# Optimization experiments

Hardware: AMD Instinct MI355X
Metric: run time of the kernel (lower is better)

## Reference

```python
import jax, jax.numpy as jnp
import numpy as np

S, V, H = 32, 16, 8            # hidden_scalars, hidden_vectors, num_heads
N, E = 10000, 100000           # nodes, edges
NRB, RH = 16, 64               # radial basis, radial MLP hidden
TH = S + 3 * V                 # packed irreps width (80)
WNUM = S * S + V * S + S * V + 2 * V * V  # TP weight_numel = 2560


def setup_inputs() -> dict:
    key = jax.random.key(0)
    ks = jax.random.split(key, 16)
    inp = {}
    inp["node_features"] = jax.random.normal(ks[0], (N, TH), jnp.float32)
    inp["edge_index"] = jax.random.randint(ks[1], (2, E), 0, N)
    inp["edge_sh"] = jax.random.normal(ks[2], (E, 4), jnp.float32)
    inp["edge_radial"] = jax.random.uniform(ks[3], (E, NRB), dtype=jnp.float32)
    inp["edge_envelope"] = jax.random.uniform(ks[4], (E,), dtype=jnp.float32)
    # radial MLP
    inp["W1"] = jax.random.normal(ks[5], (NRB, RH), jnp.float32) / np.sqrt(NRB)
    inp["b1"] = jnp.zeros((RH,), jnp.float32)
    inp["W2"] = jax.random.normal(ks[6], (RH, WNUM), jnp.float32) / np.sqrt(RH)
    inp["b2"] = jnp.zeros((WNUM,), jnp.float32)
    # attention query/key nets (scalar channels only)
    inp["Wq"] = jax.random.normal(ks[7], (S, H), jnp.float32) / np.sqrt(S)
    inp["bq"] = jnp.zeros((H,), jnp.float32)
    inp["Wk"] = jax.random.normal(ks[8], (S, H), jnp.float32) / np.sqrt(S)
    inp["bk"] = jnp.zeros((H,), jnp.float32)
    # equivariant linears (per-irrep channel mixing, e3nn style, no bias)
    inp["Wout_s"] = jax.random.normal(ks[9], (S, S), jnp.float32)
    inp["Wout_v"] = jax.random.normal(ks[10], (V, V), jnp.float32)
    inp["Wg_s"] = jax.random.normal(ks[11], (S, S + V), jnp.float32)
    inp["Wg_v"] = jax.random.normal(ks[12], (V, V), jnp.float32)
    # equivariant batch norm params
    inp["bn_ws"] = jnp.ones((S,), jnp.float32)
    inp["bn_bs"] = jnp.zeros((S,), jnp.float32)
    inp["bn_wv"] = jnp.ones((V,), jnp.float32)
    return inp


def _forward(node_features, edge_sh, edge_radial, edge_envelope,
             W1, b1, W2, b2, Wq, bq, Wk, bk,
             Wout_s, Wout_v, Wg_s, Wg_v, bn_ws, bn_bs, bn_wv, src, dst):
    # --- per-edge TP weights from radial MLP -> (E, WNUM), the big tensor ---
    tp_w = jax.nn.silu(edge_radial @ W1 + b1) @ W2 + b2
    offs = np.cumsum([0, S * S, V * S, S * V, V * V, V * V])
    WA = tp_w[:, offs[0]:offs[1]].reshape(-1, S, S)  # 0e x 0e -> 0e
    WB = tp_w[:, offs[1]:offs[2]].reshape(-1, V, S)  # 1o x 1o -> 0e
    WC = tp_w[:, offs[2]:offs[3]].reshape(-1, S, V)  # 0e x 1o -> 1o
    WD = tp_w[:, offs[3]:offs[4]].reshape(-1, V, V)  # 1o x 0e -> 1o
    WE = tp_w[:, offs[4]:offs[5]].reshape(-1, V, V)  # 1o x 1o -> 1o (cross)

    # --- gather source features, split irreps ---
    s_src = node_features[src, :S]                       # (E, S)
    v_src = node_features[src, S:].reshape(-1, V, 3)     # (E, V, 3)
    y0 = edge_sh[:, 0:1]                                 # (E, 1) l=0
    y1 = edge_sh[:, 1:4]                                 # (E, 3) l=1

    a0 = 1.0 / np.sqrt(S + V)       # path normalization, 0e output
    a1 = 1.0 / np.sqrt(S + 2 * V)   # path normalization, 1o output

    dot = (v_src * y1[:, None, :]).sum(-1) / np.sqrt(3.0)          # (E, V)
    msg_s = a0 * (jnp.einsum('es,esk->ek', s_src * y0, WA)
                  + jnp.einsum('ev,evk->ek', dot, WB))             # (E, S)
    crs = jnp.cross(v_src, y1[:, None, :]) / np.sqrt(2.0)          # (E, V, 3)
    msg_v = a1 * (jnp.einsum('es,ec,esk->ekc', s_src, y1, WC)
                  + jnp.einsum('evc,evk->ekc', v_src * y0[:, :, None], WD)
                  + jnp.einsum('evc,evk->ekc', crs, WE))           # (E, V, 3)
    messages = jnp.concatenate([msg_s, msg_v.reshape(-1, 3 * V)], axis=-1)

    # --- scatter-softmax attention over incoming edges per destination ---
    q = node_features[dst, :S] @ Wq + bq                 # (E, H)
    k = msg_s @ Wk + bk                                  # (E, H)
    logits = (q * k).sum(-1) / np.sqrt(H) + jnp.log(edge_envelope + 1e-8)
    mx = jax.ops.segment_max(logits, dst, num_segments=N)
    ex = jnp.exp(logits - mx[dst])
    den = jax.ops.segment_sum(ex, dst, num_segments=N)
    attn = ex / (den[dst] + 1e-8)                        # (E,)

    agg = jax.ops.segment_sum(attn[:, None] * messages, dst, num_segments=N)

    # --- equivariant output linear ---
    agg_s = agg[:, :S] @ Wout_s / np.sqrt(S)
    agg_v = jnp.einsum('nvc,vw->nwc', agg[:, S:].reshape(-1, V, 3), Wout_v) / np.sqrt(V)

    # --- gate ---
    gs = agg_s @ Wg_s / np.sqrt(S)                       # (N, S+V)
    gv = jnp.einsum('nvc,vw->nwc', agg_v, Wg_v) / np.sqrt(V)
    s = jax.nn.silu(gs[:, :S])
    g = jax.nn.sigmoid(gs[:, S:])
    v = g[:, :, None] * gv
    act = jnp.concatenate([s, v.reshape(-1, 3 * V)], axis=-1)

    # --- residual + equivariant batch norm ---
    x = act + node_features
    xs = x[:, :S]
    xv = x[:, S:].reshape(-1, V, 3)
    mean = xs.mean(0)
    var = xs.var(0)
    xs = (xs - mean) / jnp.sqrt(var + 1e-5) * bn_ws + bn_bs
    vn = (xv * xv).mean(-1).mean(0)                      # (V,) component norm
    xv = xv * (bn_wv / jnp.sqrt(vn + 1e-5))[None, :, None]
    return jnp.concatenate([xs, xv.reshape(-1, 3 * V)], axis=-1)


def reference(node_features, edge_index, edge_sh, edge_radial, edge_envelope,
              W1, b1, W2, b2, Wq, bq, Wk, bk,
              Wout_s, Wout_v, Wg_s, Wg_v, bn_ws, bn_bs, bn_wv):
    src, dst = edge_index[0], edge_index[1]
    return _forward(node_features, edge_sh, edge_radial, edge_envelope,
                    W1, b1, W2, b2, Wq, bq, Wk, bk,
                    Wout_s, Wout_v, Wg_s, Wg_v, bn_ws, bn_bs, bn_wv, src, dst)
```

## Files before the change

kernel.cpp:

```cpp
#include <hip/hip_runtime.h>
#include <math.h>

typedef __bf16 bf16x8 __attribute__((ext_vector_type(8)));
typedef __bf16 bf16x4 __attribute__((ext_vector_type(4)));
typedef float  f32x4  __attribute__((ext_vector_type(4)));
typedef float  f32x2  __attribute__((ext_vector_type(2)));
typedef unsigned long long u64x2 __attribute__((ext_vector_type(2)));

__device__ __forceinline__ float silu_f(float x){ return x / (1.f + __expf(-x)); }
__device__ __forceinline__ float sigm_f(float x){ return 1.f / (1.f + __expf(-x)); }

__device__ __forceinline__ float ntld_f(const float* p){
  return __builtin_nontemporal_load(p);
}
__device__ __forceinline__ float ntbf(const __bf16* p){
  unsigned short us = __builtin_nontemporal_load((const unsigned short*)p);
  union { unsigned u; float f; } cv; cv.u = ((unsigned)us) << 16;
  return cv.f;
}
__device__ __forceinline__ void nt_store_f(float* p, float v){
  __builtin_nontemporal_store(v, p);
}
__device__ __forceinline__ void nt_store_b8(__bf16* p, bf16x8 v){
  u64x2 u; __builtin_memcpy(&u, &v, 16);
// ... 133 lines not shown
  }
  for (int i = t; i < 1024; i += 256){
    int e = i >> 4, r = i & 15;
    int ec = min(e0+e, E-1);
    radl[e][r] = ntld_f(&radial[(size_t)ec*16+r]);
  }
  *(float4*)&w1l[t*4] = ((const float4*)W1)[t];
  __syncthreads();

  for (int i = t; i < 5120; i += 256){
    int e = i / 80, idx = i - e*80;
    featT[idx][e] = nf[(size_t)src_l[e]*80 + idx];
  }
  for (int i = t; i < 4096; i += 256){
    int e = i & 63, h = i >> 6;
    float acc = b1l[h];
    #pragma unroll
    for (int r = 0; r < 16; ++r) acc += radl[e][r]*w1l[r*64+h];
    u_l[e][h] = (__bf16)silu_f(acc);
  }
  __syncthreads();

  const float inv_s3 = 0.57735026918962576f;
  const float inv_s2 = 0.70710678118654752f;
  const float a0 = 0.14433756729740643f;
  const float a1 = 0.125f;

  for (int i = t; i < 3072; i += 256){
    int r = i >> 6, e = i & 63;
    float val;
    if (r < 32) val = a0 * shlT[0][e] * featT[r][e];
    else {
      int v = r - 32;
      float dot = (featT[32+v*3][e]*shlT[1][e] + featT[33+v*3][e]*shlT[2][e]
                 + featT[34+v*3][e]*shlT[3][e]) * inv_s3;
      val = a0 * dot;
    }
    cab_l[r][e] = (__bf16)val;
  }
  for (int i = t; i < 12288; i += 256){
    int e = i & 63, r = (i >> 6) & 63, c = i >> 12;
    float val;
    if (r < 32) val = a1 * shlT[1+c][e] * featT[r][e];
    else if (r < 48){
      int v = r - 32;
      val = a1 * shlT[0][e] * featT[32+v*3+c][e];
    } else {
      int v = r - 48;
      int c1 = c+1; if (c1 > 2) c1 -= 3;
      int c2 = c+2; if (c2 > 2) c2 -= 3;
      val = a1 * inv_s2 * (featT[32+v*3+c1][e]*shlT[1+c2][e]
                         - featT[32+v*3+c2][e]*shlT[1+c1][e]);
    }
    cv_l[r][c][e] = (__bf16)val;
  }
  __syncthreads();

  for (int i = t; i < 512; i += 256){
    int tl = i >> 7, rem = i & 127, k8 = rem >> 4, e = rem & 15;
    if (tg0 + tl < NT){
      bf16x8 v = *(const bf16x8*)&u_l[tl*16 + e][k8*8];
      *(bf16x8*)((char*)uG + (size_t)(tg0+tl)*2048 + k8*256 + e*16) = v;
    }
  }
  for (int i = t; i < 384; i += 256){
    int tl = i / 96, rem = i - tl*96, r = rem >> 1, h = rem & 1;
    if (tg0 + tl < NT){
      bf16x8 v = *(const bf16x8*)&cab_l[r][tl*16 + h*8];
      *(bf16x8*)((char*)cabG + (size_t)(tg0+tl)*1536 + r*32 + h*16) = v;
    }
  }
  for (int i = t; i < 1536; i += 256){
    int tl = i / 384, rem = i - tl*384, r = rem / 6, rem2 = rem - r*6,
        c = rem2 >> 1, h = rem2 & 1;
    if (tg0 + tl < NT){
      bf16x8 v = *(const bf16x8*)&cv_l[r][c][tl*16 + h*8];
      *(bf16x8*)((char*)cvG + (size_t)(tg0+tl)*6144 + r*96 + c*32 + h*16) = v;
    }
  }
}

#define LOAD_PANEL(BASE_IT, NITS) do {                                         \
    for (int idx = t; idx < (NITS)*128; idx += 512){                           \
      int itl_ = idx >> 7, rem_ = idx & 127, half_ = rem_ >> 6, o16_ = rem_ & 63;\
      *(float4*)(panel + itl_*2048 + half_*1024 + o16_*16) =                   \
        *(const float4*)(w2b + half_*163840 + (size_t)((BASE_IT)+itl_)*1024 + o16_*16);\
    }                                                                          \
    for (int i = t; i < (NITS)*16; i += 512) b2l[i] = b2[(BASE_IT)*16 + i];    \
  } while(0)

#define S_PHASE(SECOND) do {                                                   \
  int tg = wgid;                                                               \
  if (tg < NT){                                                                \
    bf16x8 uA  = *(const bf16x8*)(uGb + (size_t)tg*2048 + uOff);               \
    bf16x8 uBq = *(const bf16x8*)(uGb + (size_t)tg*2048 + 1024 + uOff);        \
    bf16x8 cb16 = *(const bf16x8*)(cabGb + (size_t)tg*1536 + lane*16);         \
    bf16x4 cb8  = *(const bf16x4*)(cabGb + (size_t)tg*1536 + 1024 + lane*8);   \
    f32x4 p0; p0[0]=0;p0[1]=0;p0[2]=0;p0[3]=0; f32x4 p1 = p0;                  \
    if (SECOND){                                                               \
      p0 = *(const f32x4*)(partU + (size_t)tg*768 + lane*8);                   \
      p1 = *(const f32x4*)(partU + (size_t)tg*768 + lane*8 + 4);               \
    }                                                                          \
    for (;;){                                                                  \
      const int tgn = tg + 2048;                                               \
      const bool hn = (tgn < NT);                                              \
      *(bf16x8*)(myCab + lane*16) = cb16;                                      \
      *(bf16x4*)(myCab + 1024 + lane*8) = cb8;                                 \
      const bf16x8 afr0 = uA, afr1 = uBq;                                      \
      bf16x8 uA_n = uA, uB_n = uBq, cb16_n = cb16; bf16x4 cb8_n = cb8;         \
      f32x4 p0_n = p0, p1_n = p1;                                              \
      if (hn){                                                                 \
        uA_n  = *(const bf16x8*)(uGb + (size_t)tgn*2048 + uOff);               \
        uB_n  = *(const bf16x8*)(uGb + (size_t)tgn*2048 + 1024 + uOff);        \
        cb16_n = *(const bf16x8*)(cabGb + (size_t)tgn*1536 + lane*16);         \
        cb8_n  = *(const bf16x4*)(cabGb + (size_t)tgn*1536 + 1024 + lane*8);   \
        if (SECOND){                                                           \
          p0_n = *(const f32x4*)(partU + (size_t)tgn*768 + lane*8);            \
          p1_n = *(const f32x4*)(partU + (size_t)tgn*768 + lane*8 + 4);        \
        }                                                                      \
      }                                                                        \
      f32x2 s0lo, s0hi, s1lo, s1hi;                                            \
      s0lo[0]=p0[0]; s0lo[1]=p0[1]; s0hi[0]=p0[2]; s0hi[1]=p0[3];              \
      s1lo[0]=p1[0]; s1lo[1]=p1[1]; s1hi[0]=p1[2]; s1hi[1]=p1[3];              \
      _Pragma("unroll 4")                                                      \
      for (int itl = 0; itl < 48; ++itl){                                      \
        bf16x8 B0 = *(const bf16x8*)(panel + itl*2048 + laneOff);              \
        bf16x8 B1 = *(const bf16x8*)(panel + itl*2048 + 1024 + laneOff);       \
        f32x4 d; d[0]=0;d[1]=0;d[2]=0;d[3]=0;                                  \
        d = __builtin_amdgcn_mfma_f32_16x16x32_bf16(afr0, B0, d, 0,0,0);       \
        d = __builtin_amdgcn_mfma_f32_16x16x32_bf16(afr1, B1, d, 0,0,0);       \
        const float bias = b2l[itl*16 + nlo];                                  \
        f32x2 bb; bb[0]=bias; bb[1]=bias;                                      \
        f32x2 dlo = __builtin_shufflevector(d,d,0,1) + bb;                     \
        f32x2 dhi = __builtin_shufflevector(d,d,2,3) + bb;                     \
        const int r = (SECOND)*24 + (itl>>1);                                  \
        bf16x4 c4 = *(const bf16x4*)(myCab + r*32 + quad*8);                   \
        if (itl & 1){ s1lo += b4lo(c4)*dlo; s1hi += b4hi(c4)*dhi; }            \
        else        { s0lo += b4lo(c4)*dlo; s0hi += b4hi(c4)*dhi; }            \
      }                                                                        \
      if (!(SECOND)){                                                          \
        f32x4 P0; P0[0]=s0lo[0]; P0[1]=s0lo[1]; P0[2]=s0hi[0]; P0[3]=s0hi[1];  \
        f32x4 P1; P1[0]=s1lo[0]; P1[1]=s1lo[1]; P1[2]=s1hi[0]; P1[3]=s1hi[1];  \
        *(f32x4*)(partU + (size_t)tg*768 + lane*8) = P0;                       \
        *(f32x4*)(partU + (size_t)tg*768 + lane*8 + 4) = P1;                   \
      } else {                                                                 \
        const int eb = quad*4;                                                 \
        myOut[(eb+0)*56 + nlo] = s0lo[0];                                      \
        myOut[(eb+1)*56 + nlo] = s0lo[1];                                      \
        myOut[(eb+2)*56 + nlo] = s0hi[0];                                      \
        myOut[(eb+3)*56 + nlo] = s0hi[1];                                      \
        myOut[(eb+0)*56 + 16+nlo] = s1lo[0];                                   \
        myOut[(eb+1)*56 + 16+nlo] = s1lo[1];                                   \
        myOut[(eb+2)*56 + 16+nlo] = s1hi[0];                                   \
        myOut[(eb+3)*56 + 16+nlo] = s1hi[1];                                   \
        const int e0e = tg*16;                                                 \
        { int e = lane>>2, seg = lane&3, eg = e0e + e;                         \
          if (eg < E){                                                         \
            f32x4 m0 = *(const f32x4*)&myOut[e*56 + seg*8];                    \
            f32x4 m1 = *(const f32x4*)&myOut[e*56 + seg*8 + 4];                \
            bf16x8 o; o[0]=(__bf16)m0[0]; o[1]=(__bf16)m0[1];                  \
            o[2]=(__bf16)m0[2]; o[3]=(__bf16)m0[3]; o[4]=(__bf16)m1[0];        \
            o[5]=(__bf16)m1[1]; o[6]=(__bf16)m1[2]; o[7]=(__bf16)m1[3];        \
            nt_store_b8(msgs + (size_t)permG[eg]*80 + seg*8, o);               \
          } }                                                                  \
        for (int r8 = 0; r8 < 2; ++r8){                                        \
          int e = r8*8 + (lane>>3), kq = lane&7, eg = e0e + e;                 \
          f32x4 ms = *(const f32x4*)&myOut[e*56 + kq*4];                       \
          int dn = ei[(size_t)E + min(eg, E-1)];                               \
          const float* kvp = kvt + (size_t)dn*32 + kq*4;                       \
          float part = ms[0]*kvp[0]+ms[1]*kvp[1]+ms[2]*kvp[2]+ms[3]*kvp[3];    \
          part += __shfl_xor(part, 1);                                         \
          part += __shfl_xor(part, 2);                                         \
          part += __shfl_xor(part, 4);                                         \
          if (kq == 0 && eg < E){                                              \
            float lg = (part + carr[dn]) * 0.35355339059327373f                \
                     + logf(ntld_f(&env[eg]) + 1e-8f);                         \
            nt_store_f(&logits_s[permG[eg]], lg);                              \
          } }                                                                  \
      }                                                                        \
      if (!hn) break;                                                          \
      uA = uA_n; uBq = uB_n; cb16 = cb16_n; cb8 = cb8_n;                       \
      p0 = p0_n; p1 = p1_n;                                                    \
      tg = tgn;                                                                \
    }                                                                          \
  }                                                                            \
} while(0)

#define V_PHASE(SECOND) do {                                                   \
  int tg = wgid;                                                               \
  if (tg < NT){                                                                \
    bf16x8 uA  = *(const bf16x8*)(uGb + (size_t)tg*2048 + uOff);               \
    bf16x8 uBq = *(const bf16x8*)(uGb + (size_t)tg*2048 + 1024 + uOff);        \
    bf16x8 cv0 = *(const bf16x8*)(cvGb + (size_t)tg*6144 + (SECOND)*3072 + lane*48);\
    bf16x8 cv1 = *(const bf16x8*)(cvGb + (size_t)tg*6144 + (SECOND)*3072 + lane*48 + 16);\
    bf16x8 cv2 = *(const bf16x8*)(cvGb + (size_t)tg*6144 + (SECOND)*3072 + lane*48 + 32);\
    f32x4 p0; p0[0]=0;p0[1]=0;p0[2]=0;p0[3]=0; f32x4 p1 = p0, p2 = p0;         \
    if (SECOND){                                                               \
      p0 = *(const f32x4*)(partU + (size_t)tg*768 + lane*12);                  \
      p1 = *(const f32x4*)(partU + (size_t)tg*768 + lane*12 + 4);              \
      p2 = *(const f32x4*)(partU + (size_t)tg*768 + lane*12 + 8);              \
    }                                                                          \
    for (;;){                                                                  \
      const int tgn = tg + 2048;                                               \
      const bool hn = (tgn < NT);                                              \
      *(bf16x8*)(myCab + lane*48)      = cv0;                                  \
      *(bf16x8*)(myCab + lane*48 + 16) = cv1;                                  \
      *(bf16x8*)(myCab + lane*48 + 32) = cv2;                                  \
      const bf16x8 afr0 = uA, afr1 = uBq;                                      \
      bf16x8 uA_n = uA, uB_n = uBq, cv0_n = cv0, cv1_n = cv1, cv2_n = cv2;     \
      f32x4 p0_n = p0, p1_n = p1, p2_n = p2;                                   \
      if (hn){                                                                 \
        uA_n = *(const bf16x8*)(uGb + (size_t)tgn*2048 + uOff);                \
        uB_n = *(const bf16x8*)(uGb + (size_t)tgn*2048 + 1024 + uOff);         \
        cv0_n = *(const bf16x8*)(cvGb + (size_t)tgn*6144 + (SECOND)*3072 + lane*48);\
        cv1_n = *(const bf16x8*)(cvGb + (size_t)tgn*6144 + (SECOND)*3072 + lane*48 + 16);\
        cv2_n = *(const bf16x8*)(cvGb + (size_t)tgn*6144 + (SECOND)*3072 + lane*48 + 32);\
        if (SECOND){                                                           \
          p0_n = *(const f32x4*)(partU + (size_t)tgn*768 + lane*12);           \
          p1_n = *(const f32x4*)(partU + (size_t)tgn*768 + lane*12 + 4);       \
          p2_n = *(const f32x4*)(partU + (size_t)tgn*768 + lane*12 + 8);       \
        }                                                                      \
      }                                                                        \
      f32x2 v0lo, v0hi, v1lo, v1hi, v2lo, v2hi;                                \
      v0lo[0]=p0[0]; v0lo[1]=p0[1]; v0hi[0]=p0[2]; v0hi[1]=p0[3];              \
      v1lo[0]=p1[0]; v1lo[1]=p1[1]; v1hi[0]=p1[2]; v1hi[1]=p1[3];              \
      v2lo[0]=p2[0]; v2lo[1]=p2[1]; v2hi[0]=p2[2]; v2hi[1]=p2[3];              \
      _Pragma("unroll 4")                                                      \
      for (int itl = 0; itl < 32; ++itl){                                      \
        bf16x8 B0 = *(const bf16x8*)(panel + itl*2048 + laneOff);              \
        bf16x8 B1 = *(const bf16x8*)(panel + itl*2048 + 1024 + laneOff);       \
        f32x4 d; d[0]=0;d[1]=0;d[2]=0;d[3]=0;                                  \
        d = __builtin_amdgcn_mfma_f32_16x16x32_bf16(afr0, B0, d, 0,0,0);       \
        d = __builtin_amdgcn_mfma_f32_16x16x32_bf16(afr1, B1, d, 0,0,0);       \
        const float bias = b2l[itl*16 + nlo];                                  \
        f32x2 bb; bb[0]=bias; bb[1]=bias;                                      \
        f32x2 dlo = __builtin_shufflevector(d,d,0,1) + bb;                     \
        f32x2 dhi = __builtin_shufflevector(d,d,2,3) + bb;                     \
        const char* cb_ = myCab + itl*96;                                      \
        bf16x4 q0 = *(const bf16x4*)(cb_ + quad*8);                            \
        bf16x4 q1 = *(const bf16x4*)(cb_ + 32 + quad*8);                       \
        bf16x4 q2 = *(const bf16x4*)(cb_ + 64 + quad*8);                       \
        v0lo += b4lo(q0)*dlo; v0hi += b4hi(q0)*dhi;                            \
        v1lo += b4lo(q1)*dlo; v1hi += b4hi(q1)*dhi;                            \
        v2lo += b4lo(q2)*dlo; v2hi += b4hi(q2)*dhi;                            \
      }                                                                        \
      if (!(SECOND)){                                                          \
        f32x4 P0; P0[0]=v0lo[0]; P0[1]=v0lo[1]; P0[2]=v0hi[0]; P0[3]=v0hi[1];  \
        f32x4 P1; P1[0]=v1lo[0]; P1[1]=v1lo[1]; P1[2]=v1hi[0]; P1[3]=v1hi[1];  \
        f32x4 P2; P2[0]=v2lo[0]; P2[1]=v2lo[1]; P2[2]=v2hi[0]; P2[3]=v2hi[1];  \
        *(f32x4*)(partU + (size_t)tg*768 + lane*12)     = P0;                  \
        *(f32x4*)(partU + (size_t)tg*768 + lane*12 + 4) = P1;                  \
        *(f32x4*)(partU + (size_t)tg*768 + lane*12 + 8) = P2;                  \
      } else {                                                                 \
        const int eb = quad*4; const int cb2 = nlo*3;                          \
        myOut[(eb+0)*56 + cb2+0] = v0lo[0];                                    \
        myOut[(eb+1)*56 + cb2+0] = v0lo[1];                                    \
        myOut[(eb+2)*56 + cb2+0] = v0hi[0];                                    \
        myOut[(eb+3)*56 + cb2+0] = v0hi[1];                                    \
        myOut[(eb+0)*56 + cb2+1] = v1lo[0];                                    \
        myOut[(eb+1)*56 + cb2+1] = v1lo[1];                                    \
        myOut[(eb+2)*56 + cb2+1] = v1hi[0];                                    \
        myOut[(eb+3)*56 + cb2+1] = v1hi[1];                                    \
        myOut[(eb+0)*56 + cb2+2] = v2lo[0];                                    \
        myOut[(eb+1)*56 + cb2+2] = v2lo[1];                                    \
        myOut[(eb+2)*56 + cb2+2] = v2hi[0];                                    \
        myOut[(eb+3)*56 + cb2+2] = v2hi[1];                                    \
        const int e0e = tg*16;                                                 \
        for (int i = lane; i < 96; i += 64){                                   \
          int e = i/6, seg = i - (i/6)*6, eg = e0e + e;                        \
          if (eg < E){                                                         \
            f32x4 m0 = *(const f32x4*)&myOut[e*56 + seg*8];                    \
            f32x4 m1 = *(const f32x4*)&myOut[e*56 + seg*8 + 4];                \
            bf16x8 o; o[0]=(__bf16)m0[0]; o[1]=(__bf16)m0[1];                  \
            o[2]=(__bf16)m0[2]; o[3]=(__bf16)m0[3]; o[4]=(__bf16)m1[0];        \
            o[5]=(__bf16)m1[1]; o[6]=(__bf16)m1[2]; o[7]=(__bf16)m1[3];        \
            nt_store_b8(msgs + (size_t)permG[eg]*80 + 32 + seg*8, o);          \
          } }                                                                  \
      }                                                                        \
      if (!hn) break;                                                          \
      uA = uA_n; uBq = uB_n; cv0 = cv0_n; cv1 = cv1_n; cv2 = cv2_n;            \
      p0 = p0_n; p1 = p1_n; p2 = p2_n;                                         \
      tg = tgn;                                                                \
    }                                                                          \
  }                                                                            \
} while(0)

__global__ void __launch_bounds__(512, 1) k_edge(
    const __bf16* __restrict__ W2t, const float* __restrict__ b2,
    const __bf16* __restrict__ uG, const __bf16* __restrict__ cabG,
    const __bf16* __restrict__ cvG, const int* __restrict__ ei,
    const int* __restrict__ permG, const float* __restrict__ kvt,
    const float* __restrict__ carr, const float* __restrict__ env,
    float* __restrict__ partU, __bf16* __restrict__ msgs,
    float* __restrict__ logits_s, int E, int NT)
{
  __shared__ __align__(16) char panel[98304];
  __shared__ __align__(16) char wstage[8][6656];
  __shared__ float b2l[768];

  const int t = threadIdx.x;
  const int lane = t & 63;
  const int wv   = t >> 6;
  const int quad = lane >> 4;
  const int nlo  = lane & 15;
  const int wgid = blockIdx.x*8 + wv;
  const int laneOff = nlo*64 + quad*16;
  const int uOff    = quad*256 + nlo*16;
  char*  myCab = wstage[wv];
  float* myOut = (float*)(wstage[wv] + 3072);
  const char* w2b   = (const char*)W2t;
  const char* uGb   = (const char*)uG;
  const char* cabGb = (const char*)cabG;
  const char* cvGb  = (const char*)cvG;

  LOAD_PANEL(0, 48);
  __syncthreads();
  S_PHASE(0);
  __syncthreads();
  LOAD_PANEL(48, 48);
  __syncthreads();
  S_PHASE(1);
  __syncthreads();
  LOAD_PANEL(96, 32);
  __syncthreads();
  V_PHASE(0);
  __syncthreads();
  LOAD_PANEL(128, 32);
  __syncthreads();
  V_PHASE(1);
}

__global__ void __launch_bounds__(256) k_agg(
    const __bf16* __restrict__ msgs, const float* __restrict__ logits_s,
    const int* __restrict__ cursor, const float* __restrict__ nf,
    const float* __restrict__ Wout_s, const float* __restrict__ Wout_v,
    const float* __restrict__ Wg_s, const float* __restrict__ Wg_v,
    float* __restrict__ xbuf, float* __restrict__ bnacc, int N)
{
  __shared__ float aggl[4][80];
  __shared__ float t1[4][96];
  __shared__ float t2[4][96];
  __shared__ float bnl[80];
  const int t = threadIdx.x, l = t & 63, wv = t >> 6;
  const int n = blockIdx.x*4 + wv;
  const bool act = (n < N);
  const int nc = act ? n : (N-1);
  if (t < 80) bnl[t] = 0.f;

  const int r0 = (nc == 0) ? 0 : cursor[nc-1];
  const int r1 = cursor[nc];
  const int deg = act ? (r1 - r0) : 0;

  float mym = -3.4e38f;
  for (int i = l; i < deg; i += 64) mym = fmaxf(mym, logits_s[r0+i]);
  #pragma unroll
  for (int s = 32; s; s >>= 1) mym = fmaxf(mym, __shfl_xor(mym, s));
  float denp = 0.f, acc0 = 0.f, acc1 = 0.f;
  for (int c0 = 0; c0 < deg; c0 += 64){
    const int len = min(64, deg - c0);
    float ex = 0.f;
    if (l < len) ex = __expf(logits_s[r0+c0+l] - mym);
    denp += ex;
    for (int j0 = 0; j0 < len; j0 += 4){
      const int jn = len - j0;
      const __bf16* base = msgs + (size_t)(r0+c0+j0)*80;
      float v0=0,v1=0,v2=0,v3=0, w0=0,w1=0,w2=0,w3=0;
      float a0_=0,a1_=0,a2_=0,a3_=0;
      v0 = ntbf(&base[l]); if (l < 16) w0 = ntbf(&base[64+l]); a0_ = __shfl(ex, j0);
      if (jn > 1){ v1 = ntbf(&base[80+l]);  if (l < 16) w1 = ntbf(&base[144+l]); a1_ = __shfl(ex, j0+1); }
      if (jn > 2){ v2 = ntbf(&base[160+l]); if (l < 16) w2 = ntbf(&base[224+l]); a2_ = __shfl(ex, j0+2); }
      if (jn > 3){ v3 = ntbf(&base[240+l]); if (l < 16) w3 = ntbf(&base[304+l]); a3_ = __shfl(ex, j0+3); }
      acc0 += a0_*v0 + a1_*v1 + a2_*v2 + a3_*v3;
      if (l < 16) acc1 += a0_*w0 + a1_*w1 + a2_*w2 + a3_*w3;
    }
  }
  #pragma unroll
  for (int s = 32; s; s >>= 1) denp += __shfl_xor(denp, s);
  const float inv = 1.f/(denp + 1e-8f);
  aggl[wv][l] = acc0 * inv;
  if (l < 16) aggl[wv][64+l] = acc1 * inv;
  __syncthreads();

  const float* arow = &aggl[wv][0];
  const float iS = 0.17677669529663687f;
  const float iV = 0.25f;
  for (int o = l; o < 80; o += 64){
    float val = 0.f;
    if (o < 32){
      for (int s = 0; s < 32; ++s) val += arow[s]*Wout_s[s*32+o];
      val *= iS;
    } else {
      int w = (o-32)/3, c = (o-32)-w*3;
// ... 129 lines not shown
```

Before: 376.2 us.

## Process two edge tiles per wave to reuse panel B-fragments, swizzle panel layout

Each wave now handles a pair of adjacent 16-edge tiles at once, so each B fragment read from the shared-memory panel feeds two MFMA chains instead of one. This halves LDS panel traffic per edge and gives the MFMA pipe two independent accumulators. The panel store layout is permuted so lane reads are contiguous by quad, which is meant to reduce LDS bank conflicts. In exchange it drops the software prefetch of the next tile, raises register pressure, and reuses the cab staging buffer as the output scratch, which shrinks the per-wave staging area.

```diff
diff --git a/kernel.cpp b/kernel.cpp
--- a/kernel.cpp
+++ b/kernel.cpp
@@ -239,205 +239,249 @@
 
 #define LOAD_PANEL(BASE_IT, NITS) do {                                         \
     for (int idx = t; idx < (NITS)*128; idx += 512){                           \
-      int itl_ = idx >> 7, rem_ = idx & 127, half_ = rem_ >> 6, o16_ = rem_ & 63;\
-      *(float4*)(panel + itl_*2048 + half_*1024 + o16_*16) =                   \
-        *(const float4*)(w2b + half_*163840 + (size_t)((BASE_IT)+itl_)*1024 + o16_*16);\
+      int itl_ = idx >> 7, rem_ = idx & 127, half_ = rem_ >> 6, r6_ = rem_ & 63;\
+      int col_ = r6_ >> 2, quad_ = r6_ & 3;                                    \
+      *(float4*)(panel + itl_*2048 + half_*1024 + quad_*256 + col_*16) =       \
+        *(const float4*)(w2b + half_*163840 + (size_t)((BASE_IT)+itl_)*1024    \
+                         + col_*64 + quad_*16);                                \
     }                                                                          \
     for (int i = t; i < (NITS)*16; i += 512) b2l[i] = b2[(BASE_IT)*16 + i];    \
   } while(0)
 
 #define S_PHASE(SECOND) do {                                                   \
-  int tg = wgid;                                                               \
-  if (tg < NT){                                                                \
-    bf16x8 uA  = *(const bf16x8*)(uGb + (size_t)tg*2048 + uOff);               \
-    bf16x8 uBq = *(const bf16x8*)(uGb + (size_t)tg*2048 + 1024 + uOff);        \
-    bf16x8 cb16 = *(const bf16x8*)(cabGb + (size_t)tg*1536 + lane*16);         \
-    bf16x4 cb8  = *(const bf16x4*)(cabGb + (size_t)tg*1536 + 1024 + lane*8);   \
-    f32x4 p0; p0[0]=0;p0[1]=0;p0[2]=0;p0[3]=0; f32x4 p1 = p0;                  \
+  for (int outer = 0; outer < 2; ++outer){                                     \
+    const int tgA = 2*wgid + outer*4096;                                       \
+    if (tgA >= NT) break;                                                      \
+    const int tgB = tgA + 1;                                                   \
+    const bool hB = (tgB < NT);                                                \
+    const int tgBc = hB ? tgB : tgA;                                           \
+    bf16x8 aA0 = *(const bf16x8*)(uGb + (size_t)tgA*2048 + uOff);              \
+    bf16x8 aA1 = *(const bf16x8*)(uGb + (size_t)tgA*2048 + 1024 + uOff);       \
+    bf16x8 aB0 = *(const bf16x8*)(uGb + (size_t)tgBc*2048 + uOff);             \
+    bf16x8 aB1 = *(const bf16x8*)(uGb + (size_t)tgBc*2048 + 1024 + uOff);      \
+    {                                                                          \
+      bf16x8 cA16 = *(const bf16x8*)(cabGb + (size_t)tgA*1536 + lane*16);      \
+      bf16x4 cA8  = *(const bf16x4*)(cabGb + (size_t)tgA*1536 + 1024 + lane*8);\
+      bf16x8 cB16 = *(const bf16x8*)(cabGb + (size_t)tgBc*1536 + lane*16);     \
+      bf16x4 cB8  = *(const bf16x4*)(cabGb + (size_t)tgBc*1536 + 1024 + lane*8);\
+      *(bf16x8*)(myCab + lane*16) = cA16;                                      \
+      *(bf16x4*)(myCab + 1024 + lane*8) = cA8;                                 \
+      *(bf16x8*)(myCab + 1536 + lane*16) = cB16;                               \
+      *(bf16x4*)(myCab + 2560 + lane*8) = cB8;                                 \
+    }                                                                          \
+    f32x2 sA0lo={0,0}, sA0hi={0,0}, sA1lo={0,0}, sA1hi={0,0};                  \
+    f32x2 sB0lo={0,0}, sB0hi={0,0}, sB1lo={0,0}, sB1hi={0,0};                  \
     if (SECOND){                                                               \
-      p0 = *(const f32x4*)(partU + (size_t)tg*768 + lane*8);                   \
-      p1 = *(const f32x4*)(partU + (size_t)tg*768 + lane*8 + 4);               \
-    }                                                                          \
-    for (;;){                                                                  \
-      const int tgn = tg + 2048;                                               \
-      const bool hn = (tgn < NT);                                              \
-      *(bf16x8*)(myCab + lane*16) = cb16;                                      \
-      *(bf16x4*)(myCab + 1024 + lane*8) = cb8;                                 \
-      const bf16x8 afr0 = uA, afr1 = uBq;                                      \
-      bf16x8 uA_n = uA, uB_n = uBq, cb16_n = cb16; bf16x4 cb8_n = cb8;         \
-      f32x4 p0_n = p0, p1_n = p1;                                              \
-      if (hn){                                                                 \
-        uA_n  = *(const bf16x8*)(uGb + (size_t)tgn*2048 + uOff);               \
-        uB_n  = *(const bf16x8*)(uGb + (size_t)tgn*2048 + 1024 + uOff);        \
-        cb16_n = *(const bf16x8*)(cabGb + (size_t)tgn*1536 + lane*16);         \
-        cb8_n  = *(const bf16x4*)(cabGb + (size_t)tgn*1536 + 1024 + lane*8);   \
-        if (SECOND){                                                           \
-          p0_n = *(const f32x4*)(partU + (size_t)tgn*768 + lane*8);            \
-          p1_n = *(const f32x4*)(partU + (size_t)tgn*768 + lane*8 + 4);        \
-        }                                                                      \
+      f32x4 p;                                                                 \
+      p = *(const f32x4*)(partU + (size_t)tgA*768 + lane*8);                   \
+      sA0lo[0]=p[0]; sA0lo[1]=p[1]; sA0hi[0]=p[2]; sA0hi[1]=p[3];              \
+      p = *(const f32x4*)(partU + (size_t)tgA*768 + lane*8 + 4);               \
+      sA1lo[0]=p[0]; sA1lo[1]=p[1]; sA1hi[0]=p[2]; sA1hi[1]=p[3];              \
+      p = *(const f32x4*)(partU + (size_t)tgBc*768 + lane*8);                  \
+      sB0lo[0]=p[0]; sB0lo[1]=p[1]; sB0hi[0]=p[2]; sB0hi[1]=p[3];              \
+      p = *(const f32x4*)(partU + (size_t)tgBc*768 + lane*8 + 4);              \
+      sB1lo[0]=p[0]; sB1lo[1]=p[1]; sB1hi[0]=p[2]; sB1hi[1]=p[3];              \
+    }                                                                          \
+    _Pragma("unroll 4")                                                        \
+    for (int itl = 0; itl < 48; ++itl){                                        \
+      bf16x8 B0 = *(const bf16x8*)(panel + itl*2048 + laneOff);                \
+      bf16x8 B1 = *(const bf16x8*)(panel + itl*2048 + 1024 + laneOff);         \
+      f32x4 dA; dA[0]=0;dA[1]=0;dA[2]=0;dA[3]=0; f32x4 dB = dA;                \
+      dA = __builtin_amdgcn_mfma_f32_16x16x32_bf16(aA0, B0, dA, 0,0,0);        \
+      dB = __builtin_amdgcn_mfma_f32_16x16x32_bf16(aB0, B0, dB, 0,0,0);        \
+      dA = __builtin_amdgcn_mfma_f32_16x16x32_bf16(aA1, B1, dA, 0,0,0);        \
+      dB = __builtin_amdgcn_mfma_f32_16x16x32_bf16(aB1, B1, dB, 0,0,0);        \
+      const float bias = b2l[itl*16 + nlo];                                    \
+      f32x2 bb; bb[0]=bias; bb[1]=bias;                                        \
+      f32x2 dAlo = __builtin_shufflevector(dA,dA,0,1) + bb;                    \
+      f32x2 dAhi = __builtin_shufflevector(dA,dA,2,3) + bb;                    \
+      f32x2 dBlo = __builtin_shufflevector(dB,dB,0,1) + bb;                    \
+      f32x2 dBhi = __builtin_shufflevector(dB,dB,2,3) + bb;                    \
+      const int r = (SECOND)*24 + (itl>>1);                                    \
+      bf16x4 cA = *(const bf16x4*)(myCab + r*32 + quad*8);                     \
+      bf16x4 cB = *(const bf16x4*)(myCab + 1536 + r*32 + quad*8);              \
+      if (itl & 1){                                                            \
+        sA1lo += b4lo(cA)*dAlo; sA1hi += b4hi(cA)*dAhi;                        \
+        sB1lo += b4lo(cB)*dBlo; sB1hi += b4hi(cB)*dBhi;                        \
+      } else {                                                                 \
+        sA0lo += b4lo(cA)*dAlo; sA0hi += b4hi(cA)*dAhi;                        \
+        sB0lo += b4lo(cB)*dBlo; sB0hi += b4hi(cB)*dBhi;                        \
       }                                                                        \
-      f32x2 s0lo, s0hi, s1lo, s1hi;                                            \
-      s0lo[0]=p0[0]; s0lo[1]=p0[1]; s0hi[0]=p0[2]; s0hi[1]=p0[3];              \
-      s1lo[0]=p1[0]; s1lo[1]=p1[1]; s1hi[0]=p1[2]; s1hi[1]=p1[3];              \
-      _Pragma("unroll 4")                                                      \
-      for (int itl = 0; itl < 48; ++itl){                                      \
-        bf16x8 B0 = *(const bf16x8*)(panel + itl*2048 + laneOff);              \
-        bf16x8 B1 = *(const bf16x8*)(panel + itl*2048 + 1024 + laneOff);       \
-        f32x4 d; d[0]=0;d[1]=0;d[2]=0;d[3]=0;                                  \
-        d = __builtin_amdgcn_mfma_f32_16x16x32_bf16(afr0, B0, d, 0,0,0);       \
-        d = __builtin_amdgcn_mfma_f32_16x16x32_bf16(afr1, B1, d, 0,0,0);       \
-        const float bias = b2l[itl*16 + nlo];                                  \
-        f32x2 bb; bb[0]=bias; bb[1]=bias;                                      \
-        f32x2 dlo = __builtin_shufflevector(d,d,0,1) + bb;                     \
-        f32x2 dhi = __builtin_shufflevector(d,d,2,3) + bb;                     \
-        const int r = (SECOND)*24 + (itl>>1);                                  \
-        bf16x4 c4 = *(const bf16x4*)(myCab + r*32 + quad*8);                   \
-        if (itl & 1){ s1lo += b4lo(c4)*dlo; s1hi += b4hi(c4)*dhi; }            \
-        else        { s0lo += b4lo(c4)*dlo; s0hi += b4hi(c4)*dhi; }            \
+    }                                                                          \
+    if (!(SECOND)){                                                            \
+      f32x4 P;                                                                 \
+      P[0]=sA0lo[0]; P[1]=sA0lo[1]; P[2]=sA0hi[0]; P[3]=sA0hi[1];              \
+      *(f32x4*)(partU + (size_t)tgA*768 + lane*8) = P;                         \
+      P[0]=sA1lo[0]; P[1]=sA1lo[1]; P[2]=sA1hi[0]; P[3]=sA1hi[1];              \
+      *(f32x4*)(partU + (size_t)tgA*768 + lane*8 + 4) = P;                     \
+      if (hB){                                                                 \
+        P[0]=sB0lo[0]; P[1]=sB0lo[1]; P[2]=sB0hi[0]; P[3]=sB0hi[1];            \
+        *(f32x4*)(partU + (size_t)tgB*768 + lane*8) = P;                       \
+        P[0]=sB1lo[0]; P[1]=sB1lo[1]; P[2]=sB1hi[0]; P[3]=sB1hi[1];            \
+        *(f32x4*)(partU + (size_t)tgB*768 + lane*8 + 4) = P;                   \
       }                                                                        \
-      if (!(SECOND)){                                                          \
-        f32x4 P0; P0[0]=s0lo[0]; P0[1]=s0lo[1]; P0[2]=s0hi[0]; P0[3]=s0hi[1];  \
-        f32x4 P1; P1[0]=s1lo[0]; P1[1]=s1lo[1]; P1[2]=s1hi[0]; P1[3]=s1hi[1];  \
-        *(f32x4*)(partU + (size_t)tg*768 + lane*8) = P0;                       \
-        *(f32x4*)(partU + (size_t)tg*768 + lane*8 + 4) = P1;                   \
-      } else {                                                                 \
-        const int eb = quad*4;                                                 \
-        myOut[(eb+0)*56 + nlo] = s0lo[0];                                      \
-        myOut[(eb+1)*56 + nlo] = s0lo[1];                                      \
-        myOut[(eb+2)*56 + nlo] = s0hi[0];                                      \
-        myOut[(eb+3)*56 + nlo] = s0hi[1];                                      \
-        myOut[(eb+0)*56 + 16+nlo] = s1lo[0];                                   \
-        myOut[(eb+1)*56 + 16+nlo] = s1lo[1];                                   \
-        myOut[(eb+2)*56 + 16+nlo] = s1hi[0];                                   \
-        myOut[(eb+3)*56 + 16+nlo] = s1hi[1];                                   \
-        const int e0e = tg*16;                                                 \
-        { int e = lane>>2, seg = lane&3, eg = e0e + e;                         \
-          if (eg < E){                                                         \
-            f32x4 m0 = *(const f32x4*)&myOut[e*56 + seg*8];                    \
-            f32x4 m1 = *(const f32x4*)&myOut[e*56 + seg*8 + 4];                \
-            bf16x8 o; o[0]=(__bf16)m0[0]; o[1]=(__bf16)m0[1];                  \
-            o[2]=(__bf16)m0[2]; o[3]=(__bf16)m0[3]; o[4]=(__bf16)m1[0];        \
-            o[5]=(__bf16)m1[1]; o[6]=(__bf16)m1[2]; o[7]=(__bf16)m1[3];        \
-            nt_store_b8(msgs + (size_t)permG[eg]*80 + seg*8, o);               \
-          } }                                                                  \
-        for (int r8 = 0; r8 < 2; ++r8){                                        \
-          int e = r8*8 + (lane>>3), kq = lane&7, eg = e0e + e;                 \
-          f32x4 ms = *(const f32x4*)&myOut[e*56 + kq*4];                       \
-          int dn = ei[(size_t)E + min(eg, E-1)];                               \
-          const float* kvp = kvt + (size_t)dn*32 + kq*4;                       \
-          float part = ms[0]*kvp[0]+ms[1]*kvp[1]+ms[2]*kvp[2]+ms[3]*kvp[3];    \
-          part += __shfl_xor(part, 1);                                         \
-          part += __shfl_xor(part, 2);                                         \
-          part += __shfl_xor(part, 4);                                         \
-          if (kq == 0 && eg < E){                                              \
-            float lg = (part + carr[dn]) * 0.35355339059327373f                \
-                     + logf(ntld_f(&env[eg]) + 1e-8f);                         \
-            nt_store_f(&logits_s[permG[eg]], lg);                              \
-          } }                                                                  \
-      }                                                                        \
-      if (!hn) break;                                                          \
-      uA = uA_n; uBq = uB_n; cb16 = cb16_n; cb8 = cb8_n;                       \
-      p0 = p0_n; p1 = p1_n;                                                    \
-      tg = tgn;                                                                \
+    } else {                                                                   \
+      const int eb = quad*4;                                                   \
+      S_FLUSH(tgA, sA0lo, sA0hi, sA1lo, sA1hi);                                \
+      if (hB){ S_FLUSH(tgB, sB0lo, sB0hi, sB1lo, sB1hi); }                     \
     }                                                                          \
   }                                                                            \
 } while(0)
 
+#define S_FLUSH(TG, S0LO, S0HI, S1LO, S1HI) do {                               \
+      myOut[(eb+0)*56 + nlo] = S0LO[0];                                        \
+      myOut[(eb+1)*56 + nlo] = S0LO[1];                                        \
+      myOut[(eb+2)*56 + nlo] = S0HI[0];                                        \
+      myOut[(eb+3)*56 + nlo] = S0HI[1];                                        \
+      myOut[(eb+0)*56 + 16+nlo] = S1LO[0];                                     \
+      myOut[(eb+1)*56 + 16+nlo] = S1LO[1];                                     \
+      myOut[(eb+2)*56 + 16+nlo] = S1HI[0];                                     \
+      myOut[(eb+3)*56 + 16+nlo] = S1HI[1];                                     \
+      const int e0e = (TG)*16;                                                 \
+      { int e = lane>>2, seg = lane&3, eg = e0e + e;                           \
+        if (eg < E){                                                           \
+          f32x4 m0 = *(const f32x4*)&myOut[e*56 + seg*8];                      \
+          f32x4 m1 = *(const f32x4*)&myOut[e*56 + seg*8 + 4];                  \
+          bf16x8 o; o[0]=(__bf16)m0[0]; o[1]=(__bf16)m0[1];                    \
+          o[2]=(__bf16)m0[2]; o[3]=(__bf16)m0[3]; o[4]=(__bf16)m1[0];          \
+          o[5]=(__bf16)m1[1]; o[6]=(__bf16)m1[2]; o[7]=(__bf16)m1[3];          \
+          nt_store_b8(msgs + (size_t)permG[eg]*80 + seg*8, o);                 \
+        } }                                                                    \
+      for (int r8 = 0; r8 < 2; ++r8){                                          \
+        int e = r8*8 + (lane>>3), kq = lane&7, eg = e0e + e;                   \
+        f32x4 ms = *(const f32x4*)&myOut[e*56 + kq*4];                         \
+        int dn = ei[(size_t)E + min(eg, E-1)];                                 \
+        const float* kvp = kvt + (size_t)dn*32 + kq*4;                         \
+        float part = ms[0]*kvp[0]+ms[1]*kvp[1]+ms[2]*kvp[2]+ms[3]*kvp[3];      \
+        part += __shfl_xor(part, 1);                                           \
+        part += __shfl_xor(part, 2);                                           \
+        part += __shfl_xor(part, 4);                                           \
+        if (kq == 0 && eg < E){                                                \
+          float lg = (part + carr[dn]) * 0.35355339059327373f                  \
+                   + logf(ntld_f(&env[eg]) + 1e-8f);                           \
+          nt_store_f(&logits_s[permG[eg]], lg);                                \
+        } }                                                                    \
+  } while(0)
+
+#define V_FLUSH(TG, V0LO, V0HI, V1LO, V1HI, V2LO, V2HI) do {                   \
+      const int cb2 = nlo*3;                                                   \
+      myOut[(eb+0)*56 + cb2+0] = V0LO[0];                                      \
+      myOut[(eb+1)*56 + cb2+0] = V0LO[1];                                      \
+      myOut[(eb+2)*56 + cb2+0] = V0HI[0];                                      \
+      myOut[(eb+3)*56 + cb2+0] = V0HI[1];                                      \
+      myOut[(eb+0)*56 + cb2+1] = V1LO[0];                                      \
+      myOut[(eb+1)*56 + cb2+1] = V1LO[1];                                      \
+      myOut[(eb+2)*56 + cb2+1] = V1HI[0];                                      \
+      myOut[(eb+3)*56 + cb2+1] = V1HI[1];                                      \
+      myOut[(eb+0)*56 + cb2+2] = V2LO[0];                                      \
+      myOut[(eb+1)*56 + cb2+2] = V2LO[1];                                      \
+      myOut[(eb+2)*56 + cb2+2] = V2HI[0];                                      \
+      myOut[(eb+3)*56 + cb2+2] = V2HI[1];                                      \
+      const int e0e = (TG)*16;                                                 \
+      for (int i = lane; i < 96; i += 64){                                     \
+        int e = i/6, seg = i - (i/6)*6, eg = e0e + e;                          \
+        if (eg < E){                                                           \
+          f32x4 m0 = *(const f32x4*)&myOut[e*56 + seg*8];                      \
+          f32x4 m1 = *(const f32x4*)&myOut[e*56 + seg*8 + 4];                  \
+          bf16x8 o; o[0]=(__bf16)m0[0]; o[1]=(__bf16)m0[1];                    \
+          o[2]=(__bf16)m0[2]; o[3]=(__bf16)m0[3]; o[4]=(__bf16)m1[0];          \
+          o[5]=(__bf16)m1[1]; o[6]=(__bf16)m1[2]; o[7]=(__bf16)m1[3];          \
+          nt_store_b8(msgs + (size_t)permG[eg]*80 + 32 + seg*8, o);            \
+        } }                                                                    \
+  } while(0)
+
 #define V_PHASE(SECOND) do {                                                   \
-  int tg = wgid;                                                               \
-  if (tg < NT){                                                                \
-    bf16x8 uA  = *(const bf16x8*)(uGb + (size_t)tg*2048 + uOff);               \
-    bf16x8 uBq = *(const bf16x8*)(uGb + (size_t)tg*2048 + 1024 + uOff);        \
-    bf16x8 cv0 = *(const bf16x8*)(cvGb + (size_t)tg*6144 + (SECOND)*3072 + lane*48);\
-    bf16x8 cv1 = *(const bf16x8*)(cvGb + (size_t)tg*6144 + (SECOND)*3072 + lane*48 + 16);\
-    bf16x8 cv2 = *(const bf16x8*)(cvGb + (size_t)tg*6144 + (SECOND)*3072 + lane*48 + 32);\
-    f32x4 p0; p0[0]=0;p0[1]=0;p0[2]=0;p0[3]=0; f32x4 p1 = p0, p2 = p0;         \
+  for (int outer = 0; outer < 2; ++outer){                                     \
+    const int tgA = 2*wgid + outer*4096;                                       \
+    if (tgA >= NT) break;                                                      \
+    const int tgB = tgA + 1;                                                   \
+    const bool hB = (tgB < NT);                                                \
+    const int tgBc = hB ? tgB : tgA;                                           \
+    bf16x8 aA0 = *(const bf16x8*)(uGb + (size_t)tgA*2048 + uOff);              \
+    bf16x8 aA1 = *(const bf16x8*)(uGb + (size_t)tgA*2048 + 1024 + uOff);       \
+    bf16x8 aB0 = *(const bf16x8*)(uGb + (size_t)tgBc*2048 + uOff);             \
+    bf16x8 aB1 = *(const bf16x8*)(uGb + (size_t)tgBc*2048 + 1024 + uOff);      \
+    {                                                                          \
+      bf16x8 c0 = *(const bf16x8*)(cvGb + (size_t)tgA*6144 + (SECOND)*3072 + lane*48);\
+      bf16x8 c1 = *(const bf16x8*)(cvGb + (size_t)tgA*6144 + (SECOND)*3072 + lane*48 + 16);\
+      bf16x8 c2 = *(const bf16x8*)(cvGb + (size_t)tgA*6144 + (SECOND)*3072 + lane*48 + 32);\
+      *(bf16x8*)(myCab + lane*48)      = c0;                                   \
+      *(bf16x8*)(myCab + lane*48 + 16) = c1;                                   \
+      *(bf16x8*)(myCab + lane*48 + 32) = c2;                                   \
+      c0 = *(const bf16x8*)(cvGb + (size_t)tgBc*6144 + (SECOND)*3072 + lane*48);\
+      c1 = *(const bf16x8*)(cvGb + (size_t)tgBc*6144 + (SECOND)*3072 + lane*48 + 16);\
+      c2 = *(const bf16x8*)(cvGb + (size_t)tgBc*6144 + (SECOND)*3072 + lane*48 + 32);\
+      *(bf16x8*)(myCab + 3072 + lane*48)      = c0;                            \
+      *(bf16x8*)(myCab + 3072 + lane*48 + 16) = c1;                            \
+      *(bf16x8*)(myCab + 3072 + lane*48 + 32) = c2;                            \
+    }                                                                          \
+    f32x2 vA0lo={0,0}, vA0hi={0,0}, vA1lo={0,0}, vA1hi={0,0}, vA2lo={0,0}, vA2hi={0,0};\
+    f32x2 vB0lo={0,0}, vB0hi={0,0}, vB1lo={0,0}, vB1hi={0,0}, vB2lo={0,0}, vB2hi={0,0};\
     if (SECOND){                                                               \
-      p0 = *(const f32x4*)(partU + (size_t)tg*768 + lane*12);                  \
-      p1 = *(const f32x4*)(partU + (size_t)tg*768 + lane*12 + 4);              \
-      p2 = *(const f32x4*)(partU + (size_t)tg*768 + lane*12 + 8);              \
-    }                                                                          \
-    for (;;){                                                                  \
-      const int tgn = tg + 2048;                                               \
-      const bool hn = (tgn < NT);                                              \
-      *(bf16x8*)(myCab + lane*48)      = cv0;                                  \
-      *(bf16x8*)(myCab + lane*48 + 16) = cv1;                                  \
-      *(bf16x8*)(myCab + lane*48 + 32) = cv2;                                  \
-      const bf16x8 afr0 = uA, afr1 = uBq;                                      \
-      bf16x8 uA_n = uA, uB_n = uBq, cv0_n = cv0, cv1_n = cv1, cv2_n = cv2;     \
-      f32x4 p0_n = p0, p1_n = p1, p2_n = p2;                                   \
-      if (hn){                                                                 \
-        uA_n = *(const bf16x8*)(uGb + (size_t)tgn*2048 + uOff);                \
-        uB_n = *(const bf16x8*)(uGb + (size_t)tgn*2048 + 1024 + uOff);         \
-        cv0_n = *(const bf16x8*)(cvGb + (size_t)tgn*6144 + (SECOND)*3072 + lane*48);\
-        cv1_n = *(const bf16x8*)(cvGb + (size_t)tgn*6144 + (SECOND)*3072 + lane*48 + 16);\
-        cv2_n = *(const bf16x8*)(cvGb + (size_t)tgn*6144 + (SECOND)*3072 + lane*48 + 32);\
-        if (SECOND){                                                           \
-          p0_n = *(const f32x4*)(partU + (size_t)tgn*768 + lane*12);           \
-          p1_n = *(const f32x4*)(partU + (size_t)tgn*768 + lane*12 + 4);       \
-          p2_n = *(const f32x4*)(partU + (size_t)tgn*768 + lane*12 + 8);       \
-        }                                                                      \
+      f32x4 p;                                                                 \
+      p = *(const f32x4*)(partU + (size_t)tgA*768 + lane*12);                  \
+      vA0lo[0]=p[0]; vA0lo[1]=p[1]; vA0hi[0]=p[2]; vA0hi[1]=p[3];              \
+      p = *(const f32x4*)(partU + (size_t)tgA*768 + lane*12 + 4);              \
+      vA1lo[0]=p[0]; vA1lo[1]=p[1]; vA1hi[0]=p[2]; vA1hi[1]=p[3];              \
+      p = *(const f32x4*)(partU + (size_t)tgA*768 + lane*12 + 8);              \
+      vA2lo[0]=p[0]; vA2lo[1]=p[1]; vA2hi[0]=p[2]; vA2hi[1]=p[3];              \
+      p = *(const f32x4*)(partU + (size_t)tgBc*768 + lane*12);                 \
+      vB0lo[0]=p[0]; vB0lo[1]=p[1]; vB0hi[0]=p[2]; vB0hi[1]=p[3];              \
+      p = *(const f32x4*)(partU + (size_t)tgBc*768 + lane*12 + 4);             \
+      vB1lo[0]=p[0]; vB1lo[1]=p[1]; vB1hi[0]=p[2]; vB1hi[1]=p[3];              \
+      p = *(const f32x4*)(partU + (size_t)tgBc*768 + lane*12 + 8);             \
+      vB2lo[0]=p[0]; vB2lo[1]=p[1]; vB2hi[0]=p[2]; vB2hi[1]=p[3];              \
+    }                                                                          \
+    _Pragma("unroll 4")                                                        \
+    for (int itl = 0; itl < 32; ++itl){                                        \
+      bf16x8 B0 = *(const bf16x8*)(panel + itl*2048 + laneOff);                \
+      bf16x8 B1 = *(const bf16x8*)(panel + itl*2048 + 1024 + laneOff);         \
+      f32x4 dA; dA[0]=0;dA[1]=0;dA[2]=0;dA[3]=0; f32x4 dB = dA;                \
+      dA = __builtin_amdgcn_mfma_f32_16x16x32_bf16(aA0, B0, dA, 0,0,0);        \
+      dB = __builtin_amdgcn_mfma_f32_16x16x32_bf16(aB0, B0, dB, 0,0,0);        \
+      dA = __builtin_amdgcn_mfma_f32_16x16x32_bf16(aA1, B1, dA, 0,0,0);        \
+      dB = __builtin_amdgcn_mfma_f32_16x16x32_bf16(aB1, B1, dB, 0,0,0);        \
+      const float bias = b2l[itl*16 + nlo];                                    \
+      f32x2 bb; bb[0]=bias; bb[1]=bias;                                        \
+      f32x2 dAlo = __builtin_shufflevector(dA,dA,0,1) + bb;                    \
+      f32x2 dAhi = __builtin_shufflevector(dA,dA,2,3) + bb;                    \
+      f32x2 dBlo = __builtin_shufflevector(dB,dB,0,1) + bb;                    \
+      f32x2 dBhi = __builtin_shufflevector(dB,dB,2,3) + bb;                    \
+      const char* cbA_ = myCab + itl*96;                                       \
+      const char* cbB_ = myCab + 3072 + itl*96;                                \
+      bf16x4 q0 = *(const bf16x4*)(cbA_ + quad*8);                             \
+      bf16x4 q1 = *(const bf16x4*)(cbA_ + 32 + quad*8);                        \
+      bf16x4 q2 = *(const bf16x4*)(cbA_ + 64 + quad*8);                        \
+      vA0lo += b4lo(q0)*dAlo; vA0hi += b4hi(q0)*dAhi;                          \
+      vA1lo += b4lo(q1)*dAlo; vA1hi += b4hi(q1)*dAhi;                          \
+      vA2lo += b4lo(q2)*dAlo; vA2hi += b4hi(q2)*dAhi;                          \
+      q0 = *(const bf16x4*)(cbB_ + quad*8);                                    \
+      q1 = *(const bf16x4*)(cbB_ + 32 + quad*8);                               \
+      q2 = *(const bf16x4*)(cbB_ + 64 + quad*8);                               \
+      vB0lo += b4lo(q0)*dBlo; vB0hi += b4hi(q0)*dBhi;                          \
+      vB1lo += b4lo(q1)*dBlo; vB1hi += b4hi(q1)*dBhi;                          \
+      vB2lo += b4lo(q2)*dBlo; vB2hi += b4hi(q2)*dBhi;                          \
+    }                                                                          \
+    if (!(SECOND)){                                                            \
+      f32x4 P;                                                                 \
+      P[0]=vA0lo[0]; P[1]=vA0lo[1]; P[2]=vA0hi[0]; P[3]=vA0hi[1];              \
+      *(f32x4*)(partU + (size_t)tgA*768 + lane*12) = P;                        \
+      P[0]=vA1lo[0]; P[1]=vA1lo[1]; P[2]=vA1hi[0]; P[3]=vA1hi[1];              \
+      *(f32x4*)(partU + (size_t)tgA*768 + lane*12 + 4) = P;                    \
+      P[0]=vA2lo[0]; P[1]=vA2lo[1]; P[2]=vA2hi[0]; P[3]=vA2hi[1];              \
+      *(f32x4*)(partU + (size_t)tgA*768 + lane*12 + 8) = P;                    \
+      if (hB){                                                                 \
+        P[0]=vB0lo[0]; P[1]=vB0lo[1]; P[2]=vB0hi[0]; P[3]=vB0hi[1];            \
+        *(f32x4*)(partU + (size_t)tgB*768 + lane*12) = P;                      \
+        P[0]=vB1lo[0]; P[1]=vB1lo[1]; P[2]=vB1hi[0]; P[3]=vB1hi[1];            \
+        *(f32x4*)(partU + (size_t)tgB*768 + lane*12 + 4) = P;                  \
+        P[0]=vB2lo[0]; P[1]=vB2lo[1]; P[2]=vB2hi[0]; P[3]=vB2hi[1];            \
+        *(f32x4*)(partU + (size_t)tgB*768 + lane*12 + 8) = P;                  \
       }                                                                        \
-      f32x2 v0lo, v0hi, v1lo, v1hi, v2lo, v2hi;                                \
-      v0lo[0]=p0[0]; v0lo[1]=p0[1]; v0hi[0]=p0[2]; v0hi[1]=p0[3];              \
-      v1lo[0]=p1[0]; v1lo[1]=p1[1]; v1hi[0]=p1[2]; v1hi[1]=p1[3];              \
-      v2lo[0]=p2[0]; v2lo[1]=p2[1]; v2hi[0]=p2[2]; v2hi[1]=p2[3];              \
-      _Pragma("unroll 4")                                                      \
-      for (int itl = 0; itl < 32; ++itl){                                      \
-        bf16x8 B0 = *(const bf16x8*)(panel + itl*2048 + laneOff);              \
-        bf16x8 B1 = *(const bf16x8*)(panel + itl*2048 + 1024 + laneOff);       \
-        f32x4 d; d[0]=0;d[1]=0;d[2]=0;d[3]=0;                                  \
-        d = __builtin_amdgcn_mfma_f32_16x16x32_bf16(afr0, B0, d, 0,0,0);       \
-        d = __builtin_amdgcn_mfma_f32_16x16x32_bf16(afr1, B1, d, 0,0,0);       \
-        const float bias = b2l[itl*16 + nlo];                                  \
-        f32x2 bb; bb[0]=bias; bb[1]=bias;                                      \
-        f32x2 dlo = __builtin_shufflevector(d,d,0,1) + bb;                     \
-        f32x2 dhi = __builtin_shufflevector(d,d,2,3) + bb;                     \
-        const char* cb_ = myCab + itl*96;                                      \
-        bf16x4 q0 = *(const bf16x4*)(cb_ + quad*8);                            \
-        bf16x4 q1 = *(const bf16x4*)(cb_ + 32 + quad*8);                       \
-        bf16x4 q2 = *(const bf16x4*)(cb_ + 64 + quad*8);                       \
-        v0lo += b4lo(q0)*dlo; v0hi += b4hi(q0)*dhi;                            \
-        v1lo += b4lo(q1)*dlo; v1hi += b4hi(q1)*dhi;                            \
-        v2lo += b4lo(q2)*dlo; v2hi += b4hi(q2)*dhi;                            \
-      }                                                                        \
-      if (!(SECOND)){                                                          \
-        f32x4 P0; P0[0]=v0lo[0]; P0[1]=v0lo[1]; P0[2]=v0hi[0]; P0[3]=v0hi[1];  \
-        f32x4 P1; P1[0]=v1lo[0]; P1[1]=v1lo[1]; P1[2]=v1hi[0]; P1[3]=v1hi[1];  \
-        f32x4 P2; P2[0]=v2lo[0]; P2[1]=v2lo[1]; P2[2]=v2hi[0]; P2[3]=v2hi[1];  \
-        *(f32x4*)(partU + (size_t)tg*768 + lane*12)     = P0;                  \
-        *(f32x4*)(partU + (size_t)tg*768 + lane*12 + 4) = P1;                  \
-        *(f32x4*)(partU + (size_t)tg*768 + lane*12 + 8) = P2;                  \
-      } else {                                                                 \
-        const int eb = quad*4; const int cb2 = nlo*3;                          \
-        myOut[(eb+0)*56 + cb2+0] = v0lo[0];                                    \
-        myOut[(eb+1)*56 + cb2+0] = v0lo[1];                                    \
-        myOut[(eb+2)*56 + cb2+0] = v0hi[0];                                    \
-        myOut[(eb+3)*56 + cb2+0] = v0hi[1];                                    \
-        myOut[(eb+0)*56 + cb2+1] = v1lo[0];                                    \
-        myOut[(eb+1)*56 + cb2+1] = v1lo[1];                                    \
-        myOut[(eb+2)*56 + cb2+1] = v1hi[0];                                    \
-        myOut[(eb+3)*56 + cb2+1] = v1hi[1];                                    \
-        myOut[(eb+0)*56 + cb2+2] = v2lo[0];                                    \
-        myOut[(eb+1)*56 + cb2+2] = v2lo[1];                                    \
-        myOut[(eb+2)*56 + cb2+2] = v2hi[0];                                    \
-        myOut[(eb+3)*56 + cb2+2] = v2hi[1];                                    \
-        const int e0e = tg*16;                                                 \
-        for (int i = lane; i < 96; i += 64){                                   \
-          int e = i/6, seg = i - (i/6)*6, eg = e0e + e;                        \
-          if (eg < E){                                                         \
-            f32x4 m0 = *(const f32x4*)&myOut[e*56 + seg*8];                    \
-            f32x4 m1 = *(const f32x4*)&myOut[e*56 + seg*8 + 4];                \
-            bf16x8 o; o[0]=(__bf16)m0[0]; o[1]=(__bf16)m0[1];                  \
-            o[2]=(__bf16)m0[2]; o[3]=(__bf16)m0[3]; o[4]=(__bf16)m1[0];        \
-            o[5]=(__bf16)m1[1]; o[6]=(__bf16)m1[2]; o[7]=(__bf16)m1[3];        \
-            nt_store_b8(msgs + (size_t)permG[eg]*80 + 32 + seg*8, o);          \
-          } }                                                                  \
-      }                                                                        \
-      if (!hn) break;                                                          \
-      uA = uA_n; uBq = uB_n; cv0 = cv0_n; cv1 = cv1_n; cv2 = cv2_n;            \
-      p0 = p0_n; p1 = p1_n; p2 = p2_n;                                         \
-      tg = tgn;                                                                \
+    } else {                                                                   \
+      const int eb = quad*4;                                                   \
+      V_FLUSH(tgA, vA0lo, vA0hi, vA1lo, vA1hi, vA2lo, vA2hi);                  \
+      if (hB){ V_FLUSH(tgB, vB0lo, vB0hi, vB1lo, vB1hi, vB2lo, vB2hi); }       \
     }                                                                          \
   }                                                                            \
 } while(0)
@@ -452,7 +496,7 @@
     float* __restrict__ logits_s, int E, int NT)
 {
   __shared__ __align__(16) char panel[98304];
-  __shared__ __align__(16) char wstage[8][6656];
+  __shared__ __align__(16) char wstage[8][6144];
   __shared__ float b2l[768];
 
   const int t = threadIdx.x;
@@ -461,10 +505,10 @@
   const int quad = lane >> 4;
   const int nlo  = lane & 15;
   const int wgid = blockIdx.x*8 + wv;
-  const int laneOff = nlo*64 + quad*16;
+  const int laneOff = quad*256 + nlo*16;
   const int uOff    = quad*256 + nlo*16;
   char*  myCab = wstage[wv];
-  float* myOut = (float*)(wstage[wv] + 3072);
+  float* myOut = (float*)wstage[wv];
   const char* w2b   = (const char*)W2t;
   const char* uGb   = (const char*)uG;
   const char* cabGb = (const char*)cabG;
```

Result: faster. 361.0 us (-4.0%).
